# Optimization experiments

Hardware: AMD Instinct MI355X
Metric: run time of the kernel (lower is better)

## Reference

```python
import jax, jax.numpy as jnp
import numpy as np

N_NODES = 50000
N_EDGES = 800000
F_IN = 128
HEADS = 4
OUT_C = 32
NEG_SLOPE = 0.2


def setup_inputs() -> dict:
    key = jax.random.key(0)
    ks = jax.random.split(key, 6)
    x = jax.random.normal(ks[0], (N_NODES, F_IN), dtype=jnp.float32)
    edge_index = jax.random.randint(ks[1], (2, N_EDGES), 0, N_NODES, dtype=jnp.int32)
    scale = 1.0 / np.sqrt(F_IN)
    W_l = jax.random.normal(ks[2], (F_IN, HEADS * OUT_C), dtype=jnp.float32) * scale
    W_r = jax.random.normal(ks[3], (F_IN, HEADS * OUT_C), dtype=jnp.float32) * scale
    b_l = jnp.zeros((HEADS * OUT_C,), dtype=jnp.float32)
    b_r = jnp.zeros((HEADS * OUT_C,), dtype=jnp.float32)
    att = jax.random.normal(ks[4], (1, HEADS, OUT_C), dtype=jnp.float32) * (1.0 / np.sqrt(OUT_C))
    bias = jnp.zeros((HEADS * OUT_C,), dtype=jnp.float32)
    return {"x": x, "edge_index": edge_index, "W_l": W_l, "b_l": b_l,
            "W_r": W_r, "b_r": b_r, "att": att, "bias": bias}


def reference(x, edge_index, W_l, b_l, W_r, b_r, att, bias):
    N = x.shape[0]
    H, C = HEADS, OUT_C
    src, dst = edge_index[0], edge_index[1]  # messages flow src(j) -> dst(i)

    x_l = (x @ W_l + b_l).reshape(N, H, C)  # Theta_t x (source/message transform)
    x_r = (x @ W_r + b_r).reshape(N, H, C)  # Theta_s x (target transform)

    # per-edge GATv2 score: a^T LeakyReLU(x_l[j] + x_r[i])
    e = x_l[src] + x_r[dst]                        # [E, H, C]
    e = jnp.where(e > 0, e, NEG_SLOPE * e)         # LeakyReLU
    alpha = jnp.sum(e * att, axis=-1)              # [E, H]

    # segment softmax over incoming edges of each dst node
    amax = jax.ops.segment_max(alpha, dst, num_segments=N)   # [N, H]
    amax = jnp.where(jnp.isfinite(amax), amax, 0.0)
    expa = jnp.exp(alpha - amax[dst])                        # [E, H]
    denom = jax.ops.segment_sum(expa, dst, num_segments=N)   # [N, H]
    alpha = expa / (denom[dst] + 1e-16)                      # [E, H]

    # scatter-aggregate messages: sum_j alpha_ij * x_l[j]
    msg = alpha[:, :, None] * x_l[src]                       # [E, H, C]
    out = jax.ops.segment_sum(msg, dst, num_segments=N)      # [N, H, C]
    out = out.reshape(N, H * C) + bias                       # concat heads + bias
    return out
```

## Files before the change

kernel.cpp:

```cpp
#include <hip/hip_runtime.h>
#include <math.h>

#define NNODES 50000
#define NEDGES 800000
#define FIN 128
#define HC 128
#define NHEADS 4
#define NEG 0.2f
#define GEMMB ((NNODES + 63) / 64)
#define HISTB ((NEDGES + 2047) / 2048)
#define ZB    ((NNODES + 255) / 256)
#define WTB   128

typedef _Float16 half8 __attribute__((ext_vector_type(8)));
typedef _Float16 half4v __attribute__((ext_vector_type(4)));
typedef float    f32x4 __attribute__((ext_vector_type(4)));

__global__ __launch_bounds__(256) void zero_wt_kernel(int* __restrict__ deg,
                                                      int* __restrict__ total,
                                                      const float* __restrict__ Wl,
                                                      const float* __restrict__ Wr,
                                                      _Float16* __restrict__ Wt) {
    int t = threadIdx.x;
    if (blockIdx.x < ZB) {
        int i = blockIdx.x * 256 + t;
        if (i < NNODES) deg[i] = 0;
        if (i == 0) *total = 0;
        return;
    }
    int flat = (blockIdx.x - ZB) * 256 + t;
    int k = flat >> 8, c = flat & 255;
    float v = (c < 128) ? Wl[(size_t)k * 128 + c] : Wr[(size_t)k * 128 + (c - 128)];
    Wt[(size_t)c * 128 + k] = (_Float16)v;
}

__global__ __launch_bounds__(256) void gemm_hist_kernel(const float* __restrict__ x,
                                                        const _Float16* __restrict__ Wt,
                                                        const float* __restrict__ bl,
                                                        const float* __restrict__ br,
                                                        _Float16* __restrict__ xlh,
                                                        _Float16* __restrict__ xrh,
                                                        const int* __restrict__ dst,
                                                        int* __restrict__ deg,
                                                        int* __restrict__ pos) {
    __shared__ _Float16 Asl[64 * 128];
    __shared__ _Float16 Bsl[256 * 128];
    int t = threadIdx.x;

    if (blockIdx.x >= GEMMB) {
        int base = (blockIdx.x - GEMMB) * 2048 + t * 8;
        if (base + 7 < NEDGES) {
            int4 d0 = *(const int4*)(dst + base);
            int4 d1 = *(const int4*)(dst + base + 4);
            int p0 = atomicAdd(&deg[d0.x], 1);
            int p1 = atomicAdd(&deg[d0.y], 1);
            int p2 = atomicAdd(&deg[d0.z], 1);
            int p3 = atomicAdd(&deg[d0.w], 1);
            int p4 = atomicAdd(&deg[d1.x], 1);
            int p5 = atomicAdd(&deg[d1.y], 1);
            int p6 = atomicAdd(&deg[d1.z], 1);
            int p7 = atomicAdd(&deg[d1.w], 1);
            *(int4*)(pos + base)     = make_int4(p0, p1, p2, p3);
            *(int4*)(pos + base + 4) = make_int4(p4, p5, p6, p7);
        } else {
            for (int i = base; i < NEDGES; ++i)
                pos[i] = atomicAdd(&deg[dst[i]], 1);
        }
        return;
    }

    int mb = blockIdx.x;
    {
        int row = t >> 2, q = t & 3;
        int node = mb * 64 + row;
        const float* xp = x + (size_t)(node < NNODES ? node : NNODES - 1) * FIN;
        #pragma unroll
        for (int uu = 0; uu < 4; ++uu) {
            int u = q * 4 + uu;
            float4 f0 = *(const float4*)(xp + u * 8);
            float4 f1 = *(const float4*)(xp + u * 8 + 4);
            half8 h = { (_Float16)f0.x, (_Float16)f0.y, (_Float16)f0.z, (_Float16)f0.w,
                        (_Float16)f1.x, (_Float16)f1.y, (_Float16)f1.z, (_Float16)f1.w };
            *(half8*)&Asl[row * 128 + (u ^ (row & 7)) * 8] = h;
        }
        #pragma unroll
        for (int i = 0; i < 16; ++i) {
            int j = t + i * 256;
            int col = j >> 4, u = j & 15;
            half8 v = *(const half8*)(Wt + (size_t)j * 8);
            *(half8*)&Bsl[col * 128 + (u ^ (col & 7)) * 8] = v;
        }
    }
    __syncthreads();

    int wv = t >> 6, lane = t & 63;
    int ln15 = lane & 15, g = lane >> 4;

    float bias_v[16];
    #pragma unroll
    for (int nb = 0; nb < 16; ++nb)
        bias_v[nb] = (nb < 8 ? bl : br)[(nb & 7) * 16 + ln15];

    half8 afrag[4];
    #pragma unroll
    for (int ks = 0; ks < 4; ++ks) {
        int rowa = wv * 16 + ln15;
        int ku = ks * 4 + g;
        afrag[ks] = *(half8*)&Asl[rowa * 128 + (ku ^ (rowa & 7)) * 8];
    }

    f32x4 acc[16];
    #pragma unroll
    for (int nb = 0; nb < 16; ++nb) acc[nb] = (f32x4){0.f, 0.f, 0.f, 0.f};

    #pragma unroll
    for (int ks = 0; ks < 4; ++ks) {
        int ku = ks * 4 + g;
        #pragma unroll
        for (int nb = 0; nb < 16; ++nb) {
            int col = nb * 16 + ln15;
            half8 bfrag = *(half8*)&Bsl[col * 128 + (ku ^ (col & 7)) * 8];
            acc[nb] = __builtin_amdgcn_mfma_f32_16x16x32_f16(afrag[ks], bfrag, acc[nb], 0, 0, 0);
        }
    }

    #pragma unroll
    for (int nb = 0; nb < 16; ++nb) {
        _Float16* oo = (nb < 8 ? xlh : xrh);
        int cm = (nb & 7) * 16 + ln15;
        #pragma unroll
        for (int i = 0; i < 4; ++i) {
            int node = mb * 64 + wv * 16 + g * 4 + i;
            if (node < NNODES)
                oo[(size_t)node * HC + cm] = (_Float16)(acc[nb][i] + bias_v[nb]);
        }
    }
}

__global__ __launch_bounds__(256) void alloc_kernel(const int* __restrict__ deg,
                                                    int* __restrict__ row_beg,
                                                    int* __restrict__ total) {
    int i = blockIdx.x * 256 + threadIdx.x;
    int lane = threadIdx.x & 63;
    int v = (i < NNODES) ? deg[i] : 0;
    int xsc = v;
    #pragma unroll
    for (int off = 1; off < 64; off <<= 1) {
        int u = __shfl_up(xsc, off);
        if (lane >= off) xsc += u;
    }
    int wbase = 0;
    if (lane == 63) wbase = atomicAdd(total, xsc);
    wbase = __shfl(wbase, 63);
    if (i < NNODES) row_beg[i] = wbase + xsc - v;
}

__global__ __launch_bounds__(256) void scatter_kernel(const int* __restrict__ src,
                                                      const int* __restrict__ dst,
                                                      const int* __restrict__ pos,
                                                      const int* __restrict__ row_beg,
                                                      int* __restrict__ csr_src) {
    int i = (blockIdx.x * 256 + threadIdx.x) * 4;
    if (i + 3 < NEDGES) {
        int4 d = *(const int4*)(dst + i);
        int4 p = *(const int4*)(pos + i);
        int4 s = *(const int4*)(src + i);
        csr_src[row_beg[d.x] + p.x] = s.x;
        csr_src[row_beg[d.y] + p.y] = s.y;
        csr_src[row_beg[d.z] + p.z] = s.z;
        csr_src[row_beg[d.w] + p.w] = s.w;
    } else {
        for (; i < NEDGES; ++i)
            csr_src[row_beg[dst[i]] + pos[i]] = src[i];
    }
}

__global__ __launch_bounds__(256) void fused_aggr_kernel(const int* __restrict__ row_beg,
                                                         const int* __restrict__ deg,
                                                         const int* __restrict__ csr_src,
                                                         const _Float16* __restrict__ xlh,
                                                         const _Float16* __restrict__ xrh,
                                                         const float* __restrict__ att,
                                                         const float* __restrict__ bias,
                                                         float* __restrict__ out) {
    int wid = threadIdx.x >> 6, lane = threadIdx.x & 63;
    int node = blockIdx.x * 4 + wid;
    if (node >= NNODES) return;
    int l32 = lane & 31, hl = lane >> 5;
    int c0 = l32 * 4;
    half4v xh = *(const half4v*)(xrh + (size_t)node * HC + c0);
    float4 xrv = make_float4((float)xh[0], (float)xh[1], (float)xh[2], (float)xh[3]);
    float4 atv = *(const float4*)(att + c0);
    float4 bv  = *(const float4*)(bias + c0);
    int pbeg = row_beg[node];
    int pend = pbeg + deg[node];
    float acc0 = 0.f, acc1 = 0.f, acc2 = 0.f, acc3 = 0.f, den = 0.f;

    #define EBODY(mh, valid)                                                   \
    {                                                                          \
        float m0 = (float)mh[0], m1 = (float)mh[1];                            \
        float m2 = (float)mh[2], m3 = (float)mh[3];                            \
        float a0 = m0 + xrv.x; a0 = a0 > 0.f ? a0 : NEG * a0;                  \
        float a1 = m1 + xrv.y; a1 = a1 > 0.f ? a1 : NEG * a1;                  \
        float a2 = m2 + xrv.z; a2 = a2 > 0.f ? a2 : NEG * a2;                  \
        float a3 = m3 + xrv.w; a3 = a3 > 0.f ? a3 : NEG * a3;                  \
        float pp = a0 * atv.x + a1 * atv.y + a2 * atv.z + a3 * atv.w;          \
        pp += __shfl_xor(pp, 1);                                               \
        pp += __shfl_xor(pp, 2);                                               \
        pp += __shfl_xor(pp, 4);                                               \
        float e = __expf(pp) * (valid);                                        \
        acc0 += e * m0; acc1 += e * m1; acc2 += e * m2; acc3 += e * m3;        \
        den += e;                                                              \
    }

    int p = pbeg;
    for (; p + 7 < pend; p += 8) {
        int s0 = csr_src[p + hl],     s1 = csr_src[p + 2 + hl];
        int s2 = csr_src[p + 4 + hl], s3 = csr_src[p + 6 + hl];
        half4v mh0 = *(const half4v*)(xlh + (size_t)s0 * HC + c0);
        half4v mh1 = *(const half4v*)(xlh + (size_t)s1 * HC + c0);
        half4v mh2 = *(const half4v*)(xlh + (size_t)s2 * HC + c0);
        half4v mh3 = *(const half4v*)(xlh + (size_t)s3 * HC + c0);
        EBODY(mh0, 1.f); EBODY(mh1, 1.f); EBODY(mh2, 1.f); EBODY(mh3, 1.f);
    }
    for (; p + 1 < pend; p += 2) {
        int s = csr_src[p + hl];
        half4v mh = *(const half4v*)(xlh + (size_t)s * HC + c0);
        EBODY(mh, 1.f);
    }
    if (p < pend) {
        int s = csr_src[p];
        half4v mh = *(const half4v*)(xlh + (size_t)s * HC + c0);
        EBODY(mh, hl ? 0.f : 1.f);
    }
    #undef EBODY

    acc0 += __shfl_xor(acc0, 32); acc1 += __shfl_xor(acc1, 32);
    acc2 += __shfl_xor(acc2, 32); acc3 += __shfl_xor(acc3, 32);
    den  += __shfl_xor(den, 32);

    if (hl == 0) {
        float inv = 1.0f / (den + 1e-16f);
        float4 o;
        o.x = acc0 * inv + bv.x;
        o.y = acc1 * inv + bv.y;
        o.z = acc2 * inv + bv.z;
        o.w = acc3 * inv + bv.w;
        *(float4*)(out + (size_t)node * HC + c0) = o;
    }
}

extern "C" void kernel_launch(void* const* d_in, const int* in_sizes, int n_in,
                              void* d_out, int out_size, void* d_ws, size_t ws_size,
                              hipStream_t stream) {
    const float* x    = (const float*)d_in[0];
    const int*   ei   = (const int*)  d_in[1];
    const float* Wl   = (const float*)d_in[2];
    const float* bl   = (const float*)d_in[3];
    const float* Wr   = (const float*)d_in[4];
    const float* br   = (const float*)d_in[5];
    const float* att  = (const float*)d_in[6];
    const float* bias = (const float*)d_in[7];
    float* out = (float*)d_out;

    _Float16* xlh = (_Float16*)d_ws;
    _Float16* xrh = xlh + (size_t)NNODES * HC;
    _Float16* Wt  = xrh + (size_t)NNODES * HC;
    int* deg     = (int*)(Wt + 256 * 128);
    int* row_beg = deg + NNODES;
    int* pos     = row_beg + NNODES;
    int* csr_src = pos + NEDGES;
    int* total   = csr_src + NEDGES;

    const int* srcp = ei;
    const int* dstp = ei + NEDGES;

    zero_wt_kernel<<<ZB + WTB, 256, 0, stream>>>(deg, total, Wl, Wr, Wt);
    gemm_hist_kernel<<<GEMMB + HISTB, 256, 0, stream>>>(x, Wt, bl, br, xlh, xrh, dstp, deg, pos);
    alloc_kernel<<<(NNODES + 255) / 256, 256, 0, stream>>>(deg, row_beg, total);
    scatter_kernel<<<(NEDGES / 4 + 255) / 256, 256, 0, stream>>>(srcp, dstp, pos, row_beg, csr_src);
    fused_aggr_kernel<<<(NNODES + 3) / 4, 256, 0, stream>>>(row_beg, deg, csr_src, xlh, xrh, att, bias, out);
}
```

Before: 131.9 us.

## Shard degree counters per edge lane, transpose GEMM output for vector stores

```diff
diff --git a/kernel.cpp b/kernel.cpp
--- a/kernel.cpp
+++ b/kernel.cpp
@@ -9,26 +9,26 @@
 #define NEG 0.2f
 #define GEMMB ((NNODES + 63) / 64)
 #define HISTB ((NEDGES + 2047) / 2048)
-#define ZB    ((NNODES + 255) / 256)
+#define ZB8   ((NNODES * 8 + 255) / 256)
 #define WTB   128
 
 typedef _Float16 half8 __attribute__((ext_vector_type(8)));
 typedef _Float16 half4v __attribute__((ext_vector_type(4)));
 typedef float    f32x4 __attribute__((ext_vector_type(4)));
 
-__global__ __launch_bounds__(256) void zero_wt_kernel(int* __restrict__ deg,
+__global__ __launch_bounds__(256) void zero_wt_kernel(int* __restrict__ deg8,
                                                       int* __restrict__ total,
                                                       const float* __restrict__ Wl,
                                                       const float* __restrict__ Wr,
                                                       _Float16* __restrict__ Wt) {
     int t = threadIdx.x;
-    if (blockIdx.x < ZB) {
+    if (blockIdx.x < ZB8) {
         int i = blockIdx.x * 256 + t;
-        if (i < NNODES) deg[i] = 0;
+        if (i < NNODES * 8) deg8[i] = 0;
         if (i == 0) *total = 0;
         return;
     }
-    int flat = (blockIdx.x - ZB) * 256 + t;
+    int flat = (blockIdx.x - ZB8) * 256 + t;
     int k = flat >> 8, c = flat & 255;
     float v = (c < 128) ? Wl[(size_t)k * 128 + c] : Wr[(size_t)k * 128 + (c - 128)];
     Wt[(size_t)c * 128 + k] = (_Float16)v;
@@ -41,7 +41,7 @@
                                                         _Float16* __restrict__ xlh,
                                                         _Float16* __restrict__ xrh,
                                                         const int* __restrict__ dst,
-                                                        int* __restrict__ deg,
+                                                        int* __restrict__ deg8,
                                                         int* __restrict__ pos) {
     __shared__ _Float16 Asl[64 * 128];
     __shared__ _Float16 Bsl[256 * 128];
@@ -52,19 +52,19 @@
         if (base + 7 < NEDGES) {
             int4 d0 = *(const int4*)(dst + base);
             int4 d1 = *(const int4*)(dst + base + 4);
-            int p0 = atomicAdd(&deg[d0.x], 1);
-            int p1 = atomicAdd(&deg[d0.y], 1);
-            int p2 = atomicAdd(&deg[d0.z], 1);
-            int p3 = atomicAdd(&deg[d0.w], 1);
-            int p4 = atomicAdd(&deg[d1.x], 1);
-            int p5 = atomicAdd(&deg[d1.y], 1);
-            int p6 = atomicAdd(&deg[d1.z], 1);
-            int p7 = atomicAdd(&deg[d1.w], 1);
+            int p0 = atomicAdd(&deg8[d0.x * 8 + 0], 1);
+            int p1 = atomicAdd(&deg8[d0.y * 8 + 1], 1);
+            int p2 = atomicAdd(&deg8[d0.z * 8 + 2], 1);
+            int p3 = atomicAdd(&deg8[d0.w * 8 + 3], 1);
+            int p4 = atomicAdd(&deg8[d1.x * 8 + 4], 1);
+            int p5 = atomicAdd(&deg8[d1.y * 8 + 5], 1);
+            int p6 = atomicAdd(&deg8[d1.z * 8 + 6], 1);
+            int p7 = atomicAdd(&deg8[d1.w * 8 + 7], 1);
             *(int4*)(pos + base)     = make_int4(p0, p1, p2, p3);
             *(int4*)(pos + base + 4) = make_int4(p4, p5, p6, p7);
         } else {
             for (int i = base; i < NEDGES; ++i)
-                pos[i] = atomicAdd(&deg[dst[i]], 1);
+                pos[i] = atomicAdd(&deg8[dst[i] * 8 + (i & 7)], 1);
         }
         return;
     }
@@ -74,21 +74,32 @@
         int row = t >> 2, q = t & 3;
         int node = mb * 64 + row;
         const float* xp = x + (size_t)(node < NNODES ? node : NNODES - 1) * FIN;
+        float4 fa[8];
+        #pragma unroll
+        for (int uu = 0; uu < 4; ++uu) {
+            fa[uu * 2]     = *(const float4*)(xp + (q * 4 + uu) * 8);
+            fa[uu * 2 + 1] = *(const float4*)(xp + (q * 4 + uu) * 8 + 4);
+        }
         #pragma unroll
         for (int uu = 0; uu < 4; ++uu) {
             int u = q * 4 + uu;
-            float4 f0 = *(const float4*)(xp + u * 8);
-            float4 f1 = *(const float4*)(xp + u * 8 + 4);
+            float4 f0 = fa[uu * 2], f1 = fa[uu * 2 + 1];
             half8 h = { (_Float16)f0.x, (_Float16)f0.y, (_Float16)f0.z, (_Float16)f0.w,
                         (_Float16)f1.x, (_Float16)f1.y, (_Float16)f1.z, (_Float16)f1.w };
             *(half8*)&Asl[row * 128 + (u ^ (row & 7)) * 8] = h;
         }
         #pragma unroll
-        for (int i = 0; i < 16; ++i) {
-            int j = t + i * 256;
-            int col = j >> 4, u = j & 15;
-            half8 v = *(const half8*)(Wt + (size_t)j * 8);
-            *(half8*)&Bsl[col * 128 + (u ^ (col & 7)) * 8] = v;
+        for (int pass = 0; pass < 2; ++pass) {
+            half8 vb[8];
+            #pragma unroll
+            for (int i = 0; i < 8; ++i)
+                vb[i] = *(const half8*)(Wt + (size_t)(t + (pass * 8 + i) * 256) * 8);
+            #pragma unroll
+            for (int i = 0; i < 8; ++i) {
+                int j = t + (pass * 8 + i) * 256;
+                int col = j >> 4, u = j & 15;
+                *(half8*)&Bsl[col * 128 + (u ^ (col & 7)) * 8] = vb[i];
+            }
         }
     }
     __syncthreads();
@@ -96,22 +107,20 @@
     int wv = t >> 6, lane = t & 63;
     int ln15 = lane & 15, g = lane >> 4;
 
-    float bias_v[16];
-    #pragma unroll
-    for (int nb = 0; nb < 16; ++nb)
-        bias_v[nb] = (nb < 8 ? bl : br)[(nb & 7) * 16 + ln15];
-
-    half8 afrag[4];
+    half8 xfrag[4];
     #pragma unroll
     for (int ks = 0; ks < 4; ++ks) {
         int rowa = wv * 16 + ln15;
         int ku = ks * 4 + g;
-        afrag[ks] = *(half8*)&Asl[rowa * 128 + (ku ^ (rowa & 7)) * 8];
+        xfrag[ks] = *(half8*)&Asl[rowa * 128 + (ku ^ (rowa & 7)) * 8];
     }
 
     f32x4 acc[16];
     #pragma unroll
-    for (int nb = 0; nb < 16; ++nb) acc[nb] = (f32x4){0.f, 0.f, 0.f, 0.f};
+    for (int nb = 0; nb < 16; ++nb) {
+        float4 b4 = *(const float4*)((nb < 8 ? bl : br) + (nb & 7) * 16 + g * 4);
+        acc[nb] = (f32x4){b4.x, b4.y, b4.z, b4.w};
+    }
 
     #pragma unroll
     for (int ks = 0; ks < 4; ++ks) {
@@ -119,30 +128,40 @@
         #pragma unroll
         for (int nb = 0; nb < 16; ++nb) {
             int col = nb * 16 + ln15;
-            half8 bfrag = *(half8*)&Bsl[col * 128 + (ku ^ (col & 7)) * 8];
-            acc[nb] = __builtin_amdgcn_mfma_f32_16x16x32_f16(afrag[ks], bfrag, acc[nb], 0, 0, 0);
-        }
-    }
-
-    #pragma unroll
-    for (int nb = 0; nb < 16; ++nb) {
-        _Float16* oo = (nb < 8 ? xlh : xrh);
-        int cm = (nb & 7) * 16 + ln15;
-        #pragma unroll
-        for (int i = 0; i < 4; ++i) {
-            int node = mb * 64 + wv * 16 + g * 4 + i;
-            if (node < NNODES)
-                oo[(size_t)node * HC + cm] = (_Float16)(acc[nb][i] + bias_v[nb]);
-        }
-    }
-}
-
-__global__ __launch_bounds__(256) void alloc_kernel(const int* __restrict__ deg,
+            half8 wfrag = *(half8*)&Bsl[col * 128 + (ku ^ (col & 7)) * 8];
+            acc[nb] = __builtin_amdgcn_mfma_f32_16x16x32_f16(wfrag, xfrag[ks], acc[nb], 0, 0, 0);
+        }
+    }
+
+    int node = mb * 64 + wv * 16 + ln15;
+    if (node < NNODES) {
+        #pragma unroll
+        for (int nb = 0; nb < 16; ++nb) {
+            _Float16* oo = (nb < 8 ? xlh : xrh);
+            half4v h = { (_Float16)acc[nb][0], (_Float16)acc[nb][1],
+                         (_Float16)acc[nb][2], (_Float16)acc[nb][3] };
+            *(half4v*)(oo + (size_t)node * HC + (nb & 7) * 16 + g * 4) = h;
+        }
+    }
+}
+
+__global__ __launch_bounds__(256) void alloc_kernel(const int* __restrict__ deg8,
                                                     int* __restrict__ row_beg,
+                                                    int* __restrict__ degsum,
+                                                    int* __restrict__ shard_beg,
                                                     int* __restrict__ total) {
     int i = blockIdx.x * 256 + threadIdx.x;
     int lane = threadIdx.x & 63;
-    int v = (i < NNODES) ? deg[i] : 0;
+    int d[8];
+    int v = 0;
+    if (i < NNODES) {
+        int4 a = *(const int4*)(deg8 + (size_t)i * 8);
+        int4 b = *(const int4*)(deg8 + (size_t)i * 8 + 4);
+        d[0] = a.x; d[1] = a.y; d[2] = a.z; d[3] = a.w;
+        d[4] = b.x; d[5] = b.y; d[6] = b.z; d[7] = b.w;
+        #pragma unroll
+        for (int s = 0; s < 8; ++s) v += d[s];
+    }
     int xsc = v;
     #pragma unroll
     for (int off = 1; off < 64; off <<= 1) {
@@ -152,31 +171,40 @@
     int wbase = 0;
     if (lane == 63) wbase = atomicAdd(total, xsc);
     wbase = __shfl(wbase, 63);
-    if (i < NNODES) row_beg[i] = wbase + xsc - v;
+    if (i < NNODES) {
+        int run = wbase + xsc - v;
+        row_beg[i] = run;
+        degsum[i] = v;
+        int sb[8];
+        #pragma unroll
+        for (int s = 0; s < 8; ++s) { sb[s] = run; run += d[s]; }
+        *(int4*)(shard_beg + (size_t)i * 8)     = make_int4(sb[0], sb[1], sb[2], sb[3]);
+        *(int4*)(shard_beg + (size_t)i * 8 + 4) = make_int4(sb[4], sb[5], sb[6], sb[7]);
+    }
 }
 
 __global__ __launch_bounds__(256) void scatter_kernel(const int* __restrict__ src,
                                                       const int* __restrict__ dst,
                                                       const int* __restrict__ pos,
-                                                      const int* __restrict__ row_beg,
+                                                      const int* __restrict__ shard_beg,
                                                       int* __restrict__ csr_src) {
     int i = (blockIdx.x * 256 + threadIdx.x) * 4;
     if (i + 3 < NEDGES) {
         int4 d = *(const int4*)(dst + i);
         int4 p = *(const int4*)(pos + i);
         int4 s = *(const int4*)(src + i);
-        csr_src[row_beg[d.x] + p.x] = s.x;
-        csr_src[row_beg[d.y] + p.y] = s.y;
-        csr_src[row_beg[d.z] + p.z] = s.z;
-        csr_src[row_beg[d.w] + p.w] = s.w;
+        csr_src[shard_beg[(size_t)d.x * 8 + ((i + 0) & 7)] + p.x] = s.x;
+        csr_src[shard_beg[(size_t)d.y * 8 + ((i + 1) & 7)] + p.y] = s.y;
+        csr_src[shard_beg[(size_t)d.z * 8 + ((i + 2) & 7)] + p.z] = s.z;
+        csr_src[shard_beg[(size_t)d.w * 8 + ((i + 3) & 7)] + p.w] = s.w;
     } else {
         for (; i < NEDGES; ++i)
-            csr_src[row_beg[dst[i]] + pos[i]] = src[i];
+            csr_src[shard_beg[(size_t)dst[i] * 8 + (i & 7)] + pos[i]] = src[i];
     }
 }
 
 __global__ __launch_bounds__(256) void fused_aggr_kernel(const int* __restrict__ row_beg,
-                                                         const int* __restrict__ deg,
+                                                         const int* __restrict__ degsum,
                                                          const int* __restrict__ csr_src,
                                                          const _Float16* __restrict__ xlh,
                                                          const _Float16* __restrict__ xrh,
@@ -193,7 +221,7 @@
     float4 atv = *(const float4*)(att + c0);
     float4 bv  = *(const float4*)(bias + c0);
     int pbeg = row_beg[node];
-    int pend = pbeg + deg[node];
+    int pend = pbeg + degsum[node];
     float acc0 = 0.f, acc1 = 0.f, acc2 = 0.f, acc3 = 0.f, den = 0.f;
 
     #define EBODY(mh, valid)                                                   \
@@ -266,18 +294,20 @@
     _Float16* xlh = (_Float16*)d_ws;
     _Float16* xrh = xlh + (size_t)NNODES * HC;
     _Float16* Wt  = xrh + (size_t)NNODES * HC;
-    int* deg     = (int*)(Wt + 256 * 128);
-    int* row_beg = deg + NNODES;
-    int* pos     = row_beg + NNODES;
-    int* csr_src = pos + NEDGES;
-    int* total   = csr_src + NEDGES;
+    int* deg8      = (int*)(Wt + 256 * 128);
+    int* row_beg   = deg8 + (size_t)NNODES * 8;
+    int* degsum    = row_beg + NNODES;
+    int* shard_beg = degsum + NNODES;
+    int* pos       = shard_beg + (size_t)NNODES * 8;
+    int* csr_src   = pos + NEDGES;
+    int* total     = csr_src + NEDGES;
 
     const int* srcp = ei;
     const int* dstp = ei + NEDGES;
 
-    zero_wt_kernel<<<ZB + WTB, 256, 0, stream>>>(deg, total, Wl, Wr, Wt);
-    gemm_hist_kernel<<<GEMMB + HISTB, 256, 0, stream>>>(x, Wt, bl, br, xlh, xrh, dstp, deg, pos);
-    alloc_kernel<<<(NNODES + 255) / 256, 256, 0, stream>>>(deg, row_beg, total);
-    scatter_kernel<<<(NEDGES / 4 + 255) / 256, 256, 0, stream>>>(srcp, dstp, pos, row_beg, csr_src);
-    fused_aggr_kernel<<<(NNODES + 3) / 4, 256, 0, stream>>>(row_beg, deg, csr_src, xlh, xrh, att, bias, out);
-}
+    zero_wt_kernel<<<ZB8 + WTB, 256, 0, stream>>>(deg8, total, Wl, Wr, Wt);
+    gemm_hist_kernel<<<GEMMB + HISTB, 256, 0, stream>>>(x, Wt, bl, br, xlh, xrh, dstp, deg8, pos);
+    alloc_kernel<<<(NNODES + 255) / 256, 256, 0, stream>>>(deg8, row_beg, degsum, shard_beg, total);
+    scatter_kernel<<<(NEDGES / 4 + 255) / 256, 256, 0, stream>>>(srcp, dstp, pos, shard_beg, csr_src);
+    fused_aggr_kernel<<<(NNODES + 3) / 4, 256, 0, stream>>>(row_beg, degsum, csr_src, xlh, xrh, att, bias, out);
+}
```

Result: slower. 145.0 us (+9.9%).

## Split GEMM by output half and separate histogram into its own kernel

Applied to the files above, without the earlier changes.

```diff
diff --git a/kernel.cpp b/kernel.cpp
--- a/kernel.cpp
+++ b/kernel.cpp
@@ -7,7 +7,7 @@
 #define HC 128
 #define NHEADS 4
 #define NEG 0.2f
-#define GEMMB ((NNODES + 63) / 64)
+#define GEMMB (((NNODES + 63) / 64) * 2)
 #define HISTB ((NEDGES + 2047) / 2048)
 #define ZB    ((NNODES + 255) / 256)
 #define WTB   128
@@ -34,72 +34,59 @@
     Wt[(size_t)c * 128 + k] = (_Float16)v;
 }
 
-__global__ __launch_bounds__(256) void gemm_hist_kernel(const float* __restrict__ x,
-                                                        const _Float16* __restrict__ Wt,
-                                                        const float* __restrict__ bl,
-                                                        const float* __restrict__ br,
-                                                        _Float16* __restrict__ xlh,
-                                                        _Float16* __restrict__ xrh,
-                                                        const int* __restrict__ dst,
-                                                        int* __restrict__ deg,
-                                                        int* __restrict__ pos) {
+__global__ __launch_bounds__(256) void gemm_kernel(const float* __restrict__ x,
+                                                   const _Float16* __restrict__ Wt,
+                                                   const float* __restrict__ bl,
+                                                   const float* __restrict__ br,
+                                                   _Float16* __restrict__ xlh,
+                                                   _Float16* __restrict__ xrh) {
     __shared__ _Float16 Asl[64 * 128];
-    __shared__ _Float16 Bsl[256 * 128];
+    __shared__ _Float16 Bsl[128 * 128];
     int t = threadIdx.x;
-
-    if (blockIdx.x >= GEMMB) {
-        int base = (blockIdx.x - GEMMB) * 2048 + t * 8;
-        if (base + 7 < NEDGES) {
-            int4 d0 = *(const int4*)(dst + base);
-            int4 d1 = *(const int4*)(dst + base + 4);
-            int p0 = atomicAdd(&deg[d0.x], 1);
-            int p1 = atomicAdd(&deg[d0.y], 1);
-            int p2 = atomicAdd(&deg[d0.z], 1);
-            int p3 = atomicAdd(&deg[d0.w], 1);
-            int p4 = atomicAdd(&deg[d1.x], 1);
-            int p5 = atomicAdd(&deg[d1.y], 1);
-            int p6 = atomicAdd(&deg[d1.z], 1);
-            int p7 = atomicAdd(&deg[d1.w], 1);
-            *(int4*)(pos + base)     = make_int4(p0, p1, p2, p3);
-            *(int4*)(pos + base + 4) = make_int4(p4, p5, p6, p7);
-        } else {
-            for (int i = base; i < NEDGES; ++i)
-                pos[i] = atomicAdd(&deg[dst[i]], 1);
-        }
-        return;
-    }
-
-    int mb = blockIdx.x;
+    int nh = blockIdx.x & 1;
+    int mb = blockIdx.x >> 1;
+
     {
         int row = t >> 2, q = t & 3;
         int node = mb * 64 + row;
         const float* xp = x + (size_t)(node < NNODES ? node : NNODES - 1) * FIN;
+        float4 fa[8];
+        #pragma unroll
+        for (int uu = 0; uu < 4; ++uu) {
+            fa[uu * 2]     = *(const float4*)(xp + (q * 4 + uu) * 8);
+            fa[uu * 2 + 1] = *(const float4*)(xp + (q * 4 + uu) * 8 + 4);
+        }
         #pragma unroll
         for (int uu = 0; uu < 4; ++uu) {
             int u = q * 4 + uu;
-            float4 f0 = *(const float4*)(xp + u * 8);
-            float4 f1 = *(const float4*)(xp + u * 8 + 4);
+            float4 f0 = fa[uu * 2], f1 = fa[uu * 2 + 1];
             half8 h = { (_Float16)f0.x, (_Float16)f0.y, (_Float16)f0.z, (_Float16)f0.w,
                         (_Float16)f1.x, (_Float16)f1.y, (_Float16)f1.z, (_Float16)f1.w };
             *(half8*)&Asl[row * 128 + (u ^ (row & 7)) * 8] = h;
         }
-        #pragma unroll
-        for (int i = 0; i < 16; ++i) {
+        const _Float16* Wh = Wt + (size_t)nh * 128 * 128;
+        half8 vb[8];
+        #pragma unroll
+        for (int i = 0; i < 8; ++i)
+            vb[i] = *(const half8*)(Wh + (size_t)(t + i * 256) * 8);
+        #pragma unroll
+        for (int i = 0; i < 8; ++i) {
             int j = t + i * 256;
             int col = j >> 4, u = j & 15;
-            half8 v = *(const half8*)(Wt + (size_t)j * 8);
-            *(half8*)&Bsl[col * 128 + (u ^ (col & 7)) * 8] = v;
+            *(half8*)&Bsl[col * 128 + (u ^ (col & 7)) * 8] = vb[i];
         }
     }
     __syncthreads();
 
     int wv = t >> 6, lane = t & 63;
     int ln15 = lane & 15, g = lane >> 4;
-
-    float bias_v[16];
-    #pragma unroll
-    for (int nb = 0; nb < 16; ++nb)
-        bias_v[nb] = (nb < 8 ? bl : br)[(nb & 7) * 16 + ln15];
+    const float* bb = nh ? br : bl;
+    _Float16*    oo = nh ? xrh : xlh;
+
+    float bias_v[8];
+    #pragma unroll
+    for (int nb = 0; nb < 8; ++nb)
+        bias_v[nb] = bb[nb * 16 + ln15];
 
     half8 afrag[4];
     #pragma unroll
@@ -109,15 +96,15 @@
         afrag[ks] = *(half8*)&Asl[rowa * 128 + (ku ^ (rowa & 7)) * 8];
     }
 
-    f32x4 acc[16];
-    #pragma unroll
-    for (int nb = 0; nb < 16; ++nb) acc[nb] = (f32x4){0.f, 0.f, 0.f, 0.f};
+    f32x4 acc[8];
+    #pragma unroll
+    for (int nb = 0; nb < 8; ++nb) acc[nb] = (f32x4){0.f, 0.f, 0.f, 0.f};
 
     #pragma unroll
     for (int ks = 0; ks < 4; ++ks) {
         int ku = ks * 4 + g;
         #pragma unroll
-        for (int nb = 0; nb < 16; ++nb) {
+        for (int nb = 0; nb < 8; ++nb) {
             int col = nb * 16 + ln15;
             half8 bfrag = *(half8*)&Bsl[col * 128 + (ku ^ (col & 7)) * 8];
             acc[nb] = __builtin_amdgcn_mfma_f32_16x16x32_f16(afrag[ks], bfrag, acc[nb], 0, 0, 0);
@@ -125,15 +112,37 @@
     }
 
     #pragma unroll
-    for (int nb = 0; nb < 16; ++nb) {
-        _Float16* oo = (nb < 8 ? xlh : xrh);
-        int cm = (nb & 7) * 16 + ln15;
+    for (int nb = 0; nb < 8; ++nb) {
+        int cm = nb * 16 + ln15;
         #pragma unroll
         for (int i = 0; i < 4; ++i) {
             int node = mb * 64 + wv * 16 + g * 4 + i;
             if (node < NNODES)
                 oo[(size_t)node * HC + cm] = (_Float16)(acc[nb][i] + bias_v[nb]);
         }
+    }
+}
+
+__global__ __launch_bounds__(256) void hist_kernel(const int* __restrict__ dst,
+                                                   int* __restrict__ deg,
+                                                   int* __restrict__ pos) {
+    int base = (blockIdx.x * 256 + threadIdx.x) * 8;
+    if (base + 7 < NEDGES) {
+        int4 d0 = *(const int4*)(dst + base);
+        int4 d1 = *(const int4*)(dst + base + 4);
+        int p0 = atomicAdd(&deg[d0.x], 1);
+        int p1 = atomicAdd(&deg[d0.y], 1);
+        int p2 = atomicAdd(&deg[d0.z], 1);
+        int p3 = atomicAdd(&deg[d0.w], 1);
+        int p4 = atomicAdd(&deg[d1.x], 1);
+        int p5 = atomicAdd(&deg[d1.y], 1);
+        int p6 = atomicAdd(&deg[d1.z], 1);
+        int p7 = atomicAdd(&deg[d1.w], 1);
+        *(int4*)(pos + base)     = make_int4(p0, p1, p2, p3);
+        *(int4*)(pos + base + 4) = make_int4(p4, p5, p6, p7);
+    } else {
+        for (int i = base; i < NEDGES; ++i)
+            pos[i] = atomicAdd(&deg[dst[i]], 1);
     }
 }
 
@@ -276,7 +285,8 @@
     const int* dstp = ei + NEDGES;
 
     zero_wt_kernel<<<ZB + WTB, 256, 0, stream>>>(deg, total, Wl, Wr, Wt);
-    gemm_hist_kernel<<<GEMMB + HISTB, 256, 0, stream>>>(x, Wt, bl, br, xlh, xrh, dstp, deg, pos);
+    gemm_kernel<<<GEMMB, 256, 0, stream>>>(x, Wt, bl, br, xlh, xrh);
+    hist_kernel<<<HISTB, 256, 0, stream>>>(dstp, deg, pos);
     alloc_kernel<<<(NNODES + 255) / 256, 256, 0, stream>>>(deg, row_beg, total);
     scatter_kernel<<<(NEDGES / 4 + 255) / 256, 256, 0, stream>>>(srcp, dstp, pos, row_beg, csr_src);
     fused_aggr_kernel<<<(NNODES + 3) / 4, 256, 0, stream>>>(row_beg, deg, csr_src, xlh, xrh, att, bias, out);
```

Result: slower. 135.8 us (+2.9%).
